# Kernel tuning notes

Measured on AMD Instinct MI355X. Metric: run time of the kernel, lower is better.

Reference implementation:

```python
import jax, jax.numpy as jnp
import numpy as np

B, H, L, C = 4, 1024, 4096, 1

def setup_inputs() -> dict:
    key = jax.random.key(0)
    kx, kk, kd = jax.random.split(key, 3)
    x = jax.random.normal(kx, (B, H, L), dtype=jnp.float32)
    k = jax.random.normal(kk, (C, H, L), dtype=jnp.float32)
    D = jax.random.normal(kd, (C, H), dtype=jnp.float32)
    return {"x": x, "k": k, "D": D}

def reference(x, k, D):
    # x: (B, H, L); k: (C, H, L); D: (C, H)
    l = x.shape[-1]
    n = 2 * l  # l_kernel + L with l_kernel = L
    k_f = jnp.fft.rfft(k, n=n)              # (C, H, n//2+1) complex
    x_f = jnp.fft.rfft(x, n=n)              # (B, H, n//2+1) complex
    y_f = jnp.einsum('bhl,chl->bchl', x_f, k_f)
    y = jnp.fft.irfft(y_f, n=n)[..., :l]    # (B, C, H, L)
    y = y + jnp.einsum('bhl,ch->bchl', x, D)
    # rearrange 'b c h l -> b (c h) l'
    b = y.shape[0]
    return y.reshape(b, -1, l)
```

## Files before the change

### kernel.cpp

```cpp
#include <hip/hip_runtime.h>

#define Bdim 4
#define Hdim 1024
#define Ldim 4096
#define NH   4096
#define NTHR 256
#define R2C  0.70710678118654752440f
#define C16C 0.92387953251128675613f
#define S16C 0.38268343236508977173f
#define INVM (1.0f / 8192.0f)

__device__ __forceinline__ int PD(int i) { return i + (i >> 4); }
__device__ __forceinline__ int bitrev12(int k) { return (int)(__brev((unsigned)k) >> 20); }
__device__ __forceinline__ int bitrev8(int k)  { return (int)(__brev((unsigned)k) >> 24); }

__device__ __forceinline__ void sincos_rev(float f, float& s, float& c) {
#if __has_builtin(__builtin_amdgcn_sinf) && __has_builtin(__builtin_amdgcn_cosf)
    s = __builtin_amdgcn_sinf(f);
    c = __builtin_amdgcn_cosf(f);
#else
    __sincosf(f * 6.28318530717958647692f, &s, &c);
#endif
}

__device__ __forceinline__ float2 cadd(float2 a, float2 b) { return make_float2(a.x + b.x, a.y + b.y); }
__device__ __forceinline__ float2 csub(float2 a, float2 b) { return make_float2(a.x - b.x, a.y - b.y); }
__device__ __forceinline__ float2 cmul(float2 a, float2 b) {
    return make_float2(a.x * b.x - a.y * b.y, a.x * b.y + a.y * b.x);
}
__device__ __forceinline__ float2 mulc(float2 a, float cr, float ci) {
    return make_float2(a.x * cr - a.y * ci, a.x * ci + a.y * cr);
}
__device__ __forceinline__ float2 cmuli(float2 a)    { return make_float2(-a.y, a.x); }
__device__ __forceinline__ float2 cmulnegi(float2 a) { return make_float2(a.y, -a.x); }
__device__ __forceinline__ float2 conjf(float2 a)    { return make_float2(a.x, -a.y); }

#define FBF(i, jj, tw)      { float2 u_ = e[i]; float2 d_ = csub(u_, e[jj]); e[i] = cadd(u_, e[jj]); e[jj] = cmul(d_, tw); }
#define FBFC(i, jj, cr, ci) { float2 u_ = e[i]; float2 d_ = csub(u_, e[jj]); e[i] = cadd(u_, e[jj]); e[jj] = mulc(d_, cr, ci); }
#define FBFN(i, jj)         { float2 u_ = e[i]; float2 d_ = csub(u_, e[jj]); e[i] = cadd(u_, e[jj]); e[jj] = cmulnegi(d_); }
#define BFU(i, jj)          { float2 u_ = e[i]; float2 v_ = e[jj]; e[i] = cadd(u_, v_); e[jj] = csub(u_, v_); }
#define IBF(i, jj, tw)      { float2 tv_ = cmul(e[jj], tw); float2 u_ = e[i]; e[i] = cadd(u_, tv_); e[jj] = csub(u_, tv_); }
#define IBFC(i, jj, cr, ci) { float2 tv_ = mulc(e[jj], cr, ci); float2 u_ = e[i]; e[i] = cadd(u_, tv_); e[jj] = csub(u_, tv_); }
#define IBFI(i, jj)         { float2 tv_ = cmuli(e[jj]); float2 u_ = e[i]; e[i] = cadd(u_, tv_); e[jj] = csub(u_, tv_); }

__device__ __forceinline__ void fwd16_tail(float2 e[16], float2 w) {
    float2 w2 = cmul(w, w);
    float2 u1 = mulc(w2, R2C, -R2C);
    float2 u2 = cmulnegi(w2);
    float2 u3 = cmulnegi(u1);
    FBF(0,4,w2) FBF(1,5,u1) FBF(2,6,u2) FBF(3,7,u3)
    FBF(8,12,w2) FBF(9,13,u1) FBF(10,14,u2) FBF(11,15,u3)
    float2 w4 = cmul(w2, w2);
    float2 w4n = cmulnegi(w4);
    FBF(0,2,w4) FBF(1,3,w4n) FBF(4,6,w4) FBF(5,7,w4n)
    FBF(8,10,w4) FBF(9,11,w4n) FBF(12,14,w4) FBF(13,15,w4n)
    float2 w8 = cmul(w4, w4);
    FBF(0,1,w8) FBF(2,3,w8) FBF(4,5,w8) FBF(6,7,w8)
    FBF(8,9,w8) FBF(10,11,w8) FBF(12,13,w8) FBF(14,15,w8)
}
__device__ __forceinline__ void fwd16(float2 e[16], float2 w) {
    float2 t1 = mulc(w, C16C, -S16C);
    float2 t2 = mulc(w, R2C, -R2C);
    float2 t3 = mulc(w, S16C, -C16C);
    float2 t4 = cmulnegi(w);
    float2 t5 = cmulnegi(t1);
    float2 t6 = cmulnegi(t2);
    float2 t7 = cmulnegi(t3);
    FBF(0,8,w) FBF(1,9,t1) FBF(2,10,t2) FBF(3,11,t3)
    FBF(4,12,t4) FBF(5,13,t5) FBF(6,14,t6) FBF(7,15,t7)
    fwd16_tail(e, w);
}
__device__ __forceinline__ void fwd16_zero(float2 e[16], float2 w) {
    float2 t1 = mulc(w, C16C, -S16C);
    float2 t2 = mulc(w, R2C, -R2C);
    float2 t3 = mulc(w, S16C, -C16C);
    e[8]  = cmul(e[0], w);
    e[9]  = cmul(e[1], t1);
    e[10] = cmul(e[2], t2);
    e[11] = cmul(e[3], t3);
    e[12] = cmul(e[4], cmulnegi(w));
    e[13] = cmul(e[5], cmulnegi(t1));
    e[14] = cmul(e[6], cmulnegi(t2));
    e[15] = cmul(e[7], cmulnegi(t3));
    fwd16_tail(e, w);
}
__device__ __forceinline__ void fwd16_unit(float2 e[16]) {
    BFU(0,8)
    FBFC(1,9,   C16C, -S16C)
    FBFC(2,10,  R2C,  -R2C)
    FBFC(3,11,  S16C, -C16C)
    FBFN(4,12)
    FBFC(5,13, -S16C, -C16C)
    FBFC(6,14, -R2C,  -R2C)
    FBFC(7,15, -C16C, -S16C)
    BFU(0,4)  FBFC(1,5,  R2C, -R2C) FBFN(2,6)   FBFC(3,7,  -R2C, -R2C)
    BFU(8,12) FBFC(9,13, R2C, -R2C) FBFN(10,14) FBFC(11,15,-R2C, -R2C)
    BFU(0,2)  FBFN(1,3)  BFU(4,6)   FBFN(5,7)
    BFU(8,10) FBFN(9,11) BFU(12,14) FBFN(13,15)
    BFU(0,1) BFU(2,3) BFU(4,5) BFU(6,7) BFU(8,9) BFU(10,11) BFU(12,13) BFU(14,15)
}

__device__ __forceinline__ void inv16_head(float2 e[16], float2 v) {
    float2 v2 = cmul(v, v);
    float2 v4 = cmul(v2, v2);
    float2 v8 = cmul(v4, v4);
    IBF(0,1,v8) IBF(2,3,v8) IBF(4,5,v8) IBF(6,7,v8)
    IBF(8,9,v8) IBF(10,11,v8) IBF(12,13,v8) IBF(14,15,v8)
    float2 v4i = cmuli(v4);
    IBF(0,2,v4) IBF(1,3,v4i) IBF(4,6,v4) IBF(5,7,v4i)
    IBF(8,10,v4) IBF(9,11,v4i) IBF(12,14,v4) IBF(13,15,v4i)
    float2 p1 = mulc(v2, R2C, R2C);
    float2 p2 = cmuli(v2);
    float2 p3 = cmuli(p1);
    IBF(0,4,v2) IBF(1,5,p1) IBF(2,6,p2) IBF(3,7,p3)
    IBF(8,12,v2) IBF(9,13,p1) IBF(10,14,p2) IBF(11,15,p3)
}
__device__ __forceinline__ void inv16(float2 e[16], float2 v) {
    inv16_head(e, v);
    float2 s1 = mulc(v, C16C, S16C);
    float2 s2 = mulc(v, R2C, R2C);
    float2 s3 = mulc(v, S16C, C16C);
    IBF(0,8,v) IBF(1,9,s1) IBF(2,10,s2) IBF(3,11,s3)
    float2 s4 = cmuli(v);
    float2 s5 = cmuli(s1);
    float2 s6 = cmuli(s2);
    float2 s7 = cmuli(s3);
    IBF(4,12,s4) IBF(5,13,s5) IBF(6,14,s6) IBF(7,15,s7)
}
__device__ __forceinline__ void inv16_low(float2 e[16], float2 v) {
    inv16_head(e, v);
    float2 s1 = mulc(v, C16C, S16C);
    float2 s2 = mulc(v, R2C, R2C);
    float2 s3 = mulc(v, S16C, C16C);
    e[0] = cadd(e[0], cmul(e[8],  v));
    e[1] = cadd(e[1], cmul(e[9],  s1));
    e[2] = cadd(e[2], cmul(e[10], s2));
    e[3] = cadd(e[3], cmul(e[11], s3));
    e[4] = cadd(e[4], cmul(e[12], cmuli(v)));
    e[5] = cadd(e[5], cmul(e[13], cmuli(s1)));
    e[6] = cadd(e[6], cmul(e[14], cmuli(s2)));
    e[7] = cadd(e[7], cmul(e[15], cmuli(s3)));
}
__device__ __forceinline__ void inv16_unit(float2 e[16]) {
    BFU(0,1) BFU(2,3) BFU(4,5) BFU(6,7) BFU(8,9) BFU(10,11) BFU(12,13) BFU(14,15)
    BFU(0,2)  IBFI(1,3)  BFU(4,6)   IBFI(5,7)
    BFU(8,10) IBFI(9,11) BFU(12,14) IBFI(13,15)
    BFU(0,4)  IBFC(1,5,  R2C, R2C) IBFI(2,6)   IBFC(3,7,  -R2C, R2C)
    BFU(8,12) IBFC(9,13, R2C, R2C) IBFI(10,14) IBFC(11,15,-R2C, R2C)
    BFU(0,8)
    IBFC(1,9,   C16C, S16C)
    IBFC(2,10,  R2C,  R2C)
    IBFC(3,11,  S16C, C16C)
    IBFI(4,12)
    IBFC(5,13, -S16C, C16C)
    IBFC(6,14, -R2C,  R2C)
    IBFC(7,15, -C16C, S16C)
}

__device__ __forceinline__ constexpr int jp0_of(int j) {
    constexpr int tbl[16] = {0,1,3,2,7,6,5,4,15,14,13,12,11,10,9,8};
    return tbl[j];
}

__global__ __launch_bounds__(NTHR)
void kspec_kernel(const float* __restrict__ kin, float4* __restrict__ kw)
{
    __shared__ float2 A[NH + (NH >> 4)];
    const int t = threadIdx.x;
    const int h = blockIdx.x;
    const float2* krow2 = (const float2*)(kin + (size_t)h * Ldim);

    {
        float2 w; sincos_rev(-(float)t * (1.0f / 4096.0f), w.y, w.x);
        float2 e[16];
        #pragma unroll
        for (int j = 0; j < 8; ++j) e[j] = krow2[t + 256 * j];
        fwd16_zero(e, w);
        const int pg = t + (t >> 4);
        #pragma unroll
        for (int j = 0; j < 16; ++j) A[pg + 272 * j] = e[j];
    }
    __syncthreads();
    {
        float2 w; sincos_rev(-(float)(t & 15) * (1.0f / 256.0f), w.y, w.x);
        const int base = ((t >> 4) << 8) | (t & 15);
        const int pb = base + (base >> 4);
        float2 e[16];
        #pragma unroll
        for (int j = 0; j < 16; ++j) e[j] = A[pb + 17 * j];
        fwd16(e, w);
        #pragma unroll
        for (int j = 0; j < 16; ++j) A[pb + 17 * j] = e[j];
    }
    __syncthreads();
    {
        const int baseA = 17 * t;
        float2 e[16];
        #pragma unroll
        for (int j = 0; j < 16; ++j) e[j] = A[baseA + j];
        fwd16_unit(e);
        #pragma unroll
        for (int j = 0; j < 16; ++j) A[baseA + j] = e[j];
    }
    __syncthreads();
    float4* kwp = kw + (size_t)h * NH;
    #pragma unroll 1
    for (int q = 0; q < 16; ++q) {
        const int p = t + 256 * q;
        const int k = bitrev12(p);
        if (k == 0) {
            float2 Z0 = A[0];
            float B0 = (Z0.x + Z0.y) * INVM;
            float BN = (Z0.x - Z0.y) * INVM;
            kwp[0] = make_float4(B0 + BN, 0.0f, 0.0f, B0 - BN);
        } else {
            const int kc = 4096 - k;
            float2 Zk = A[PD(p)];
            float2 Zc = A[PD(bitrev12(kc))];
            float s_, c_;
            sincos_rev(-(float)k * (1.0f / 8192.0f), s_, c_);
            float2 P = make_float2(0.5f * (1.0f + s_), -0.5f * c_);
            float2 Q = make_float2(0.5f * (1.0f - s_),  0.5f * c_);
            float2 Bfk = cadd(cmul(P, Zk), cmul(Q, conjf(Zc)));
            float2 Bfc = cadd(cmul(conjf(P), Zc), cmul(conjf(Q), conjf(Zk)));
            Bfk.x *= INVM; Bfk.y *= INVM; Bfc.x *= INVM; Bfc.y *= INVM;
            float2 cBfc = conjf(Bfc);
            const float ap_ = 1.0f + s_, am_ = 1.0f - s_;
            float2 G1 = make_float2(ap_ * Bfk.x + am_ * cBfc.x,
                                    ap_ * Bfk.y + am_ * cBfc.y);
            float2 d1 = csub(Bfk, cBfc);
            float2 G2 = make_float2(-c_ * d1.y, c_ * d1.x);
            kwp[p] = make_float4(G1.x, G1.y, G2.x, G2.y);
        }
    }
}

__global__ __launch_bounds__(NTHR)
void conv_kernel(const float* __restrict__ x, const float4* __restrict__ kw,
                 const float* __restrict__ Din, float* __restrict__ out)
{
    __shared__ float2 A[NH + (NH >> 4)];
    const int t = threadIdx.x;
    const int Dd = blockIdx.x;
    const int bid = ((Dd & 7) << 9) | (Dd >> 3);
    const int h = bid >> 2;
    const int b = bid & 3;
    const float Dh = Din[h];
    const float2* xrow2 = (const float2*)(x + ((size_t)b * Hdim + h) * Ldim);
    float2* orow2 = (float2*)(out + ((size_t)b * Hdim + h) * Ldim);

    float2 xr[8];
    {
        float2 w; sincos_rev(-(float)t * (1.0f / 4096.0f), w.y, w.x);
        float2 e[16];
        #pragma unroll
        for (int j = 0; j < 8; ++j) { xr[j] = xrow2[t + 256 * j]; e[j] = xr[j]; }
        fwd16_zero(e, w);
        const int pg = t + (t >> 4);
        #pragma unroll
        for (int j = 0; j < 16; ++j) A[pg + 272 * j] = e[j];
    }
    __syncthreads();
    {
        float2 w; sincos_rev(-(float)(t & 15) * (1.0f / 256.0f), w.y, w.x);
        const int base = ((t >> 4) << 8) | (t & 15);
        const int pb = base + (base >> 4);
        float2 e[16];
        #pragma unroll
        for (int j = 0; j < 16; ++j) e[j] = A[pb + 17 * j];
        fwd16(e, w);
        #pragma unroll
        for (int j = 0; j < 16; ++j) A[pb + 17 * j] = e[j];
    }
    __syncthreads();
    {
        const int a = t;
        const int s = bitrev8(a);
        const int ap = bitrev8((256 - s) & 255);
        const int baseA = 17 * a;
        const int baseB = 17 * ap;
        float2 za[16], zb[16];
        #pragma unroll
        for (int j = 0; j < 16; ++j) za[j] = A[baseA + j];
        #pragma unroll
        for (int j = 0; j < 16; ++j) zb[j] = A[baseB + j];
        fwd16_unit(za);
        fwd16_unit(zb);
        const float4* Gp = kw + (size_t)h * NH + (a << 4);
        const bool a0 = (a == 0);
        #pragma unroll
        for (int j = 0; j < 16; ++j) {
            float4 g = Gp[j];
            float2 zpart = a0 ? zb[jp0_of(j)] : zb[15 - j];
            za[j] = cadd(cmul(make_float2(g.x, g.y), za[j]),
                         cmul(make_float2(g.z, g.w), conjf(zpart)));
        }
        inv16_unit(za);
        #pragma unroll
        for (int j = 0; j < 16; ++j) A[baseA + j] = za[j];
    }
    __syncthreads();
    {
        float2 v; sincos_rev((float)(t & 15) * (1.0f / 256.0f), v.y, v.x);
        const int base = ((t >> 4) << 8) | (t & 15);
        const int pb = base + (base >> 4);
        float2 e[16];
        #pragma unroll
        for (int j = 0; j < 16; ++j) e[j] = A[pb + 17 * j];
        inv16(e, v);
        #pragma unroll
        for (int j = 0; j < 16; ++j) A[pb + 17 * j] = e[j];
    }
    __syncthreads();
    {
        float2 v; sincos_rev((float)t * (1.0f / 4096.0f), v.y, v.x);
        const int pg = t + (t >> 4);
        float2 e[16];
        #pragma unroll
        for (int j = 0; j < 16; ++j) e[j] = A[pg + 272 * j];
        inv16_low(e, v);
        #pragma unroll
        for (int j = 0; j < 8; ++j) {
            orow2[t + 256 * j] = make_float2(e[j].x + Dh * xr[j].x,
                                             e[j].y + Dh * xr[j].y);
        }
    }
}

extern "C" void kernel_launch(void* const* d_in, const int* in_sizes, int n_in,
                              void* d_out, int out_size, void* d_ws, size_t ws_size,
                              hipStream_t stream)
{
    const float* x  = (const float*)d_in[0];
    const float* k  = (const float*)d_in[1];
    const float* D  = (const float*)d_in[2];
    float* out = (float*)d_out;
    float4* kw = (float4*)d_ws;

    hipLaunchKernelGGL(kspec_kernel, dim3(Hdim), dim3(NTHR), 0, stream, k, kw);
    hipLaunchKernelGGL(conv_kernel, dim3(Bdim * Hdim), dim3(NTHR), 0, stream,
                       x, kw, D, out);
}
```

Measured before the change: 95.45 us.

## Pair mirror-bin threads via lane shuffle instead of redundant second FFT

Threads are remapped with a permutation (sigma_of) so each thread's mirror-frequency partner sits in the adjacent lane. The partner's spectrum then comes from __shfl_xor instead of having every thread reload and recompute a second 16-point FFT. The precomputed kernel weights are stored in the same thread-major order, so each thread reads a contiguous 16-entry chunk. This roughly halves the LDS reads and FFT arithmetic in the pointwise stage. In exchange it adds shuffles and special cases for threads 0 and 1.

Measured after the change: 151.5 us. 1.59x slower.

```diff
diff --git a/kernel.cpp b/kernel.cpp
--- a/kernel.cpp
+++ b/kernel.cpp
@@ -12,7 +12,13 @@
 
 __device__ __forceinline__ int PD(int i) { return i + (i >> 4); }
 __device__ __forceinline__ int bitrev12(int k) { return (int)(__brev((unsigned)k) >> 20); }
-__device__ __forceinline__ int bitrev8(int k)  { return (int)(__brev((unsigned)k) >> 24); }
+
+__device__ __forceinline__ int sigma_of(int t) {
+    if (t < 2) return t;
+    const int p = t >> 1;
+    const int msbv = 1 << (31 - __clz((unsigned)p));
+    return (t & 1) ? (5 * msbv - 1 - p) : (p + msbv);
+}
 
 __device__ __forceinline__ void sincos_rev(float f, float& s, float& c) {
 #if __has_builtin(__builtin_amdgcn_sinf) && __has_builtin(__builtin_amdgcn_cosf)
@@ -204,18 +210,20 @@
     }
     __syncthreads();
     float4* kwp = kw + (size_t)h * NH;
+    const int a = sigma_of(t);
     #pragma unroll 1
-    for (int q = 0; q < 16; ++q) {
-        const int p = t + 256 * q;
-        const int k = bitrev12(p);
+    for (int j = 0; j < 16; ++j) {
+        const int pos = 16 * a + j;
+        const int k = bitrev12(pos);
+        float4 gout;
         if (k == 0) {
             float2 Z0 = A[0];
             float B0 = (Z0.x + Z0.y) * INVM;
             float BN = (Z0.x - Z0.y) * INVM;
-            kwp[0] = make_float4(B0 + BN, 0.0f, 0.0f, B0 - BN);
+            gout = make_float4(B0 + BN, 0.0f, 0.0f, B0 - BN);
         } else {
             const int kc = 4096 - k;
-            float2 Zk = A[PD(p)];
+            float2 Zk = A[PD(pos)];
             float2 Zc = A[PD(bitrev12(kc))];
             float s_, c_;
             sincos_rev(-(float)k * (1.0f / 8192.0f), s_, c_);
@@ -230,8 +238,9 @@
                                     ap_ * Bfk.y + am_ * cBfc.y);
             float2 d1 = csub(Bfk, cBfc);
             float2 G2 = make_float2(-c_ * d1.y, c_ * d1.x);
-            kwp[p] = make_float4(G1.x, G1.y, G2.x, G2.y);
+            gout = make_float4(G1.x, G1.y, G2.x, G2.y);
         }
+        kwp[(t << 4) + j] = gout;
     }
 }
 
@@ -274,26 +283,28 @@
     }
     __syncthreads();
     {
-        const int a = t;
-        const int s = bitrev8(a);
-        const int ap = bitrev8((256 - s) & 255);
+        const int a = sigma_of(t);
         const int baseA = 17 * a;
-        const int baseB = 17 * ap;
-        float2 za[16], zb[16];
+        float2 za[16];
         #pragma unroll
         for (int j = 0; j < 16; ++j) za[j] = A[baseA + j];
-        #pragma unroll
-        for (int j = 0; j < 16; ++j) zb[j] = A[baseB + j];
         fwd16_unit(za);
-        fwd16_unit(zb);
-        const float4* Gp = kw + (size_t)h * NH + (a << 4);
-        const bool a0 = (a == 0);
+        float2 zp[16];
+        #pragma unroll
+        for (int j = 0; j < 16; ++j) {
+            float sx = __shfl_xor(za[15 - j].x, 1);
+            float sy = __shfl_xor(za[15 - j].y, 1);
+            float2 v = make_float2(sx, sy);
+            if (t == 0) v = za[jp0_of(j)];
+            else if (t == 1) v = za[15 - j];
+            zp[j] = v;
+        }
+        const float4* Gp = kw + (size_t)h * NH + (t << 4);
         #pragma unroll
         for (int j = 0; j < 16; ++j) {
             float4 g = Gp[j];
-            float2 zpart = a0 ? zb[jp0_of(j)] : zb[15 - j];
             za[j] = cadd(cmul(make_float2(g.x, g.y), za[j]),
-                         cmul(make_float2(g.z, g.w), conjf(zpart)));
+                         cmul(make_float2(g.z, g.w), conjf(zp[j])));
         }
         inv16_unit(za);
         #pragma unroll
```
